# Performance work log

Measured on AMD Instinct MI355X. Metric: run time of the kernel, lower is better.

Reference implementation:

```python
import jax, jax.numpy as jnp
import numpy as np

N = 10000   # total nodes (hits) across events
K = 16      # n_neighbours (excluding self)
F = 64      # input feature dim
H = 128     # hidden width (hard-coded in module)
BIG = 1e9

def _selu(x):
    return jax.nn.selu(x)

def _glorot(key, shape):
    fan_in, fan_out = shape
    s = jnp.sqrt(2.0 / (fan_in + fan_out)).astype(jnp.float32)
    return jax.random.normal(key, shape, dtype=jnp.float32) * s

def setup_inputs() -> dict:
    key = jax.random.key(0)
    ks = jax.random.split(key, 10)
    h = jax.random.normal(ks[0], (N, F), dtype=jnp.float32)
    coords = jax.random.normal(ks[1], (N, 3), dtype=jnp.float32)
    row_splits = jnp.array([0, N // 2, N], dtype=jnp.int32)
    return {
        'h': h, 'coords': coords, 'row_splits': row_splits,
        'W_e1': _glorot(ks[2], (2 * F + 1, H)), 'b_e1': jnp.zeros((H,), jnp.float32),
        'W_e2': _glorot(ks[3], (H, H)), 'b_e2': jnp.zeros((H,), jnp.float32),
        'W_c1': _glorot(ks[4], (H, H)), 'b_c1': jnp.zeros((H,), jnp.float32),
        'W_c2': _glorot(ks[5], (H, 1)), 'b_c2': jnp.zeros((1,), jnp.float32),
        'W_n1': _glorot(ks[6], (H + F, H)), 'b_n1': jnp.zeros((H,), jnp.float32),
        'W_n2': _glorot(ks[7], (H, H)), 'b_n2': jnp.zeros((H,), jnp.float32),
    }

def _knn(coords, row_splits):
    # segment id per node from row_splits (constant)
    n = coords.shape[0]
    seg = jnp.searchsorted(row_splits, jnp.arange(n), side='right') - 1
    nrm = jnp.sum(coords * coords, axis=1)                      # [N]
    d2 = nrm[:, None] + nrm[None, :] - 2.0 * (coords @ coords.T)
    d2 = jnp.maximum(d2, 0.0)
    same = seg[:, None] == seg[None, :]
    d2 = jnp.where(same, d2, BIG)
    negd, idx = jax.lax.top_k(-d2, K + 1)                       # includes self (dist 0)
    dist = jnp.maximum(-negd, 0.0)                              # [N, K+1]
    return idx, dist

def reference(h, coords, row_splits, W_e1, b_e1, W_e2, b_e2, W_c1, b_c1, W_c2, b_c2, W_n1, b_n1, W_n2, b_n2):
    idx, dist = _knn(coords, row_splits)                        # [N,K+1]
    nidx = idx[:, 1:]                                           # [N,K]
    d = dist[:, 1:]                                             # [N,K]
    coord_diff = coords[:, None, :] - coords[idx[:, 1:]]        # [N,K,3]

    hg = h[idx]                                                 # SelectWithDefault gather [N,K+1,F]
    h_self = hg[:, 0, :]                                        # [N,F]
    h_node = jnp.broadcast_to(h_self[:, None, :], (h.shape[0], K, F)).reshape(-1, F)
    h_neig = hg[:, 1:, :].reshape(-1, F)
    radial0 = d.reshape(-1, 1)

    e = jnp.concatenate([radial0, h_node, h_neig], axis=1)      # [N*K, 2F+1]
    e = _selu(e @ W_e1 + b_e1)
    e = _selu(e @ W_e2 + b_e2)                                  # [N*K, H]

    c = _selu(e @ W_c1 + b_c1)
    w = (c @ W_c2 + b_c2).reshape(-1, K, 1)                     # [N,K,1]
    trans = jnp.mean(coord_diff * w, axis=1)                    # [N,3]
    coords_new = coords + trans

    e_sum = e.reshape(-1, K, H).sum(axis=1)                     # [N,H]
    agg = jnp.concatenate([e_sum, h_self], axis=1)              # [N,H+F]
    out = _selu(agg @ W_n1 + b_n1) @ W_n2 + b_n2                # [N,H]
    return out, coords_new, nidx, d
```

## Files before the change

kernel.cpp:

```cpp
#include <hip/hip_runtime.h>
#include <cstdint>

#define KNB 16
#define FDIM 64
#define HDIM 128
#define NPB 8
#define ROWS 128
#define CMAXW 80
#define PADN 5120

typedef unsigned long long ull;
typedef _Float16 f16x8 __attribute__((ext_vector_type(8)));
typedef float    f32x16 __attribute__((ext_vector_type(16)));

__device__ __forceinline__ float selu_f(float x){
    const float a = 1.6732632423543772f, s = 1.0507009873554805f;
    return x > 0.f ? s * x : s * a * (__expf(x) - 1.0f);
}

__device__ __forceinline__ unsigned int pack2(float a, float b){
    union { _Float16 h[2]; unsigned int u; } t;
    t.h[0] = (_Float16)a; t.h[1] = (_Float16)b;
    return t.u;
}

__device__ __forceinline__ f16x8 ldfrag4(const unsigned int* p, unsigned int di){
    union { uint4 q; f16x8 v; } t;
    t.q = *(const uint4*)(p + di);
    return t.v;
}

template<int CTRL>
__device__ __forceinline__ unsigned int dppmin_u32(unsigned int v){
    unsigned int t = (unsigned int)__builtin_amdgcn_update_dpp(
        -1, (int)v, CTRL, 0xF, 0xF, false);
    return t < v ? t : v;
}
__device__ __forceinline__ unsigned int wave_min_u32(unsigned int v){
    v = dppmin_u32<0x111>(v);
    v = dppmin_u32<0x112>(v);
    v = dppmin_u32<0x114>(v);
    v = dppmin_u32<0x118>(v);
    v = dppmin_u32<0x142>(v);
    v = dppmin_u32<0x143>(v);
    return (unsigned int)__builtin_amdgcn_readlane((int)v, 63);
}

__global__ __launch_bounds__(256) void prep_kernel(
    const float* __restrict__ We1, const float* __restrict__ We2,
    const float* __restrict__ Wc1, _Float16* __restrict__ WT,
    const float* __restrict__ coords, float4* __restrict__ c4, int n, int npad)
{
    int b = blockIdx.x;
    if (b < 192){
        int id = b * 256 + threadIdx.x;
        int m  = id >> 14;
        int r  = id & 16383;
        int nn = (r >> 7) & 127;
        int k  = r & 127;
        float v;
        if (m == 0)      v = We1[(k + 1) * 128 + nn];
        else if (m == 1) v = We2[k * 128 + nn];
        else             v = Wc1[k * 128 + nn];
        WT[m * 16384 + nn * 128 + k] = (_Float16)v;
    } else {
        int i = (b - 192) * 256 + threadIdx.x;
        if (i < n){
            float x = coords[3*i], y = coords[3*i+1], z = coords[3*i+2];
            float nrm = __fadd_rn(__fadd_rn(__fmul_rn(x,x), __fmul_rn(y,y)), __fmul_rn(z,z));
            c4[i] = make_float4(x, y, z, nrm);
        } else if (i < npad){
            c4[i] = make_float4(0.f, 0.f, 0.f, __uint_as_float(0x7f800000u));
        }
    }
}

__global__ __launch_bounds__(256) void knn_kernel(
    const float4* __restrict__ c4,
    const int* __restrict__ row_splits, int nseg, int n,
    int* __restrict__ nidx, float* __restrict__ ndist, int* __restrict__ idx0,
    float* __restrict__ out_nidx, float* __restrict__ out_d)
{
    const int lane = threadIdx.x & 63;
    const int wid  = threadIdx.x >> 6;
    const int i    = blockIdx.x * 4 + wid;
    if (i >= n) return;

    int lo = 0, hi = n;
    for (int s = 0; s < nseg; ++s){
        int a = row_splits[s], b = row_splits[s+1];
        if (i >= a && i < b){ lo = a; hi = b; }
    }

    const float4 ci = c4[i];
    const float cx = ci.x, cy = ci.y, cz = ci.z, nrmi = ci.w;

    const int jbase = lo + lane;
    const float FINF = __uint_as_float(0x7f800000u);

    ull m1 = ~0ull, m2 = ~0ull, m3 = ~0ull;

    #define D2_OF(v) __fsub_rn(__fadd_rn(nrmi, (v).w), __fmul_rn(2.0f, \
        __fadd_rn(__fadd_rn(__fmul_rn(cx,(v).x), __fmul_rn(cy,(v).y)), __fmul_rn(cz,(v).z))))
    #define INS(kk) { \
        ull n1 = (kk) < m1 ? (kk) : m1; \
        ull t1 = (kk) < m1 ? m1 : (kk); \
        ull n2 = t1 < m2 ? t1 : m2; \
        ull t2 = t1 < m2 ? m2 : t1; \
        ull n3 = t2 < m3 ? t2 : m3; \
        m1 = n1; m2 = n2; m3 = n3; }

    for (int c0 = 0; c0 < CMAXW; c0 += 8){
        float4 v[8]; int jj[8];
        #pragma unroll
        for (int q = 0; q < 8; ++q){
            jj[q] = jbase + (c0 + q)*64;
            v[q]  = c4[jj[q]];
        }
        #pragma unroll
        for (int q = 0; q < 8; ++q){
            float dv = (jj[q] < hi) ? fmaxf(D2_OF(v[q]), 0.0f) : FINF;
            ull kk = (((ull)__float_as_uint(dv)) << 32) | (unsigned int)jj[q];
            INS(kk)
        }
    }
    int vcnt = 3;

    for (int r = 0; r < KNB + 1; ++r){
        unsigned int h32 = (unsigned int)(m1 >> 32);
        unsigned int l32 = (unsigned int)m1;
        unsigned int wmd = wave_min_u32(h32);
        unsigned int jm  = (h32 == wmd) ? l32 : 0xFFFFFFFFu;
        unsigned int wmj = wave_min_u32(jm);

        bool own = (h32 == wmd) && (l32 == wmj);
        bool need = false;
        if (own){
            int   j  = (int)wmj;
            float dv = __uint_as_float(wmd);
            if (r == 0){
                idx0[i] = j;
            } else {
                int rr = r - 1;
                nidx[i*KNB + rr]     = j;
                ndist[i*KNB + rr]    = dv;
                out_nidx[i*KNB + rr] = (float)j;
                out_d[i*KNB + rr]    = dv;
            }
            m1 = m2; m2 = m3; m3 = ~0ull;
            need = (--vcnt == 0);
        }

        if (__ballot((int)need)){
            if (need){
                ull b = (((ull)wmd) << 32) | wmj;
                m1 = m2 = m3 = ~0ull;
                for (int c = 0; c < CMAXW; ++c){
                    int j = jbase + c*64;
                    float4 v = c4[j];
                    float dv = (j < hi) ? fmaxf(D2_OF(v), 0.0f) : FINF;
                    ull kk = (((ull)__float_as_uint(dv)) << 32) | (unsigned int)j;
                    kk = kk > b ? kk : ~0ull;
                    INS(kk)
                }
                vcnt = 3;
            }
        }
    }
    #undef INS
    #undef D2_OF
}

#define SWZ(row, d) ((unsigned int)(d) ^ ((((unsigned int)(row)) & 7u) << 2))

__global__ __launch_bounds__(256, 2) void egcn_node_kernel(
    const float* __restrict__ h, const float* __restrict__ coords,
    const int* __restrict__ nidx, const float* __restrict__ ndist,
    const int* __restrict__ idx0, const _Float16* __restrict__ WTg,
    const float* __restrict__ W_e1, const float* __restrict__ b_e1,
    const float* __restrict__ b_e2, const float* __restrict__ b_c1,
    const float* __restrict__ W_c2, const float* __restrict__ b_c2,
    float* __restrict__ aggout, float* __restrict__ out_coords, int n)
{
    __shared__ __attribute__((aligned(16))) _Float16 Act[ROWS * 128];
    __shared__ __attribute__((aligned(16))) unsigned int wt[ROWS * 64];
    __shared__ float agg[NPB][HDIM];
    __shared__ float dls[ROWS];
    __shared__ int   nb[ROWS];
    __shared__ int   j0s[NPB];
    __shared__ float wedge[ROWS];

    const int g0  = blockIdx.x * NPB;
    const int tid = threadIdx.x;
    const int lane = tid & 63, wid = tid >> 6;
    const int ln31 = lane & 31, grp = lane >> 5;
    const int rt  = wid;

    if (tid < ROWS){
        int e = min(g0*KNB + tid, n*KNB - 1);
        nb[tid]  = nidx[e];
        dls[tid] = ndist[e];
    }
    if (tid < NPB) j0s[tid] = idx0[min(g0 + tid, n - 1)];
    __syncthreads();

    unsigned int* actd = (unsigned int*)Act;

    {
        int r = tid >> 1, half = tid & 1;
        const float4* hs = (const float4*)(h + (size_t)j0s[r >> 4] * FDIM + half*32);
        const float4* hn = (const float4*)(h + (size_t)nb[r] * FDIM + half*32);
        unsigned int rb = (unsigned int)r * 64;
        uint4 buf[4];
        #pragma unroll
        for (int q = 0; q < 4; ++q){
            float4 a = hs[2*q], b = hs[2*q+1];
            buf[q].x = pack2(a.x,a.y); buf[q].y = pack2(a.z,a.w);
            buf[q].z = pack2(b.x,b.y); buf[q].w = pack2(b.z,b.w);
        }
        #pragma unroll
        for (int q = 0; q < 4; ++q)
            *(uint4*)(actd + rb + SWZ(r, half*16 + 4*q)) = buf[q];
        #pragma unroll
        for (int q = 0; q < 4; ++q){
            float4 a = hn[2*q], b = hn[2*q+1];
            buf[q].x = pack2(a.x,a.y); buf[q].y = pack2(a.z,a.w);
            buf[q].z = pack2(b.x,b.y); buf[q].w = pack2(b.z,b.w);
        }
        #pragma unroll
        for (int q = 0; q < 4; ++q)
            *(uint4*)(actd + rb + SWZ(r, 32 + half*16 + 4*q)) = buf[q];
    }
    auto stage_wt = [&](const _Float16* Wg){
        int nr = tid >> 1, half = tid & 1;
        const uint4* src = (const uint4*)(Wg + nr * 128 + half*64);
        unsigned int rb = (unsigned int)nr * 64;
        #pragma unroll
        for (int q = 0; q < 8; ++q)
            *(uint4*)(wt + rb + SWZ(nr, half*32 + q*4)) = src[q];
    };
    stage_wt(WTg);
    __syncthreads();

    const unsigned int sA    = ((unsigned int)ln31 & 7u) << 2;
    const unsigned int aRow  = (unsigned int)(rt*32 + ln31) * 64;
    const unsigned int bRow0 = (unsigned int)(ln31      ) * 64;
    const unsigned int bRow1 = (unsigned int)(32  + ln31) * 64;
    const unsigned int bRow2 = (unsigned int)(64  + ln31) * 64;
    const unsigned int bRow3 = (unsigned int)(96  + ln31) * 64;

    auto gemm4 = [&](f32x16& A0, f32x16& A1, f32x16& A2, f32x16& A3){
        #pragma unroll
        for (int ks = 0; ks < 8; ++ks){
            const unsigned int o = ((unsigned int)(ks*8 + grp*4)) ^ sA;
            f16x8 af = ldfrag4(actd, aRow + o);
            A0 = __builtin_amdgcn_mfma_f32_32x32x16_f16(af, ldfrag4(wt, bRow0 + o), A0, 0, 0, 0);
            A1 = __builtin_amdgcn_mfma_f32_32x32x16_f16(af, ldfrag4(wt, bRow1 + o), A1, 0, 0, 0);
            A2 = __builtin_amdgcn_mfma_f32_32x32x16_f16(af, ldfrag4(wt, bRow2 + o), A2, 0, 0, 0);
            A3 = __builtin_amdgcn_mfma_f32_32x32x16_f16(af, ldfrag4(wt, bRow3 + o), A3, 0, 0, 0);
        }
    };
    #define ROW_OF(reg) (rt*32 + ((reg)&3) + 8*((reg)>>2) + 4*grp)

    auto act_st = [&](int row, int col, float v){
        unsigned int d = SWZ(row, col >> 1);
        Act[row*128 + (d << 1) + (col & 1)] = (_Float16)v;
    };

    {
        float w00 = W_e1[ln31],      w01 = W_e1[32+ln31];
        float w02 = W_e1[64+ln31],   w03 = W_e1[96+ln31];
        float bz0 = b_e1[ln31],      bz1 = b_e1[32+ln31];
        float bz2 = b_e1[64+ln31],   bz3 = b_e1[96+ln31];
        f32x16 a0, a1, a2, a3;
        #pragma unroll
        for (int reg = 0; reg < 16; ++reg){
            float dv = dls[ROW_OF(reg)];
            a0[reg] = fmaf(dv, w00, bz0);
            a1[reg] = fmaf(dv, w01, bz1);
            a2[reg] = fmaf(dv, w02, bz2);
            a3[reg] = fmaf(dv, w03, bz3);
        }
        gemm4(a0, a1, a2, a3);
        __syncthreads();
        #pragma unroll
        for (int reg = 0; reg < 16; ++reg){
            int row = ROW_OF(reg);
            act_st(row, ln31,      selu_f(a0[reg]));
            act_st(row, 32 + ln31, selu_f(a1[reg]));
            act_st(row, 64 + ln31, selu_f(a2[reg]));
            act_st(row, 96 + ln31, selu_f(a3[reg]));
        }
        stage_wt(WTg + 16384);
        __syncthreads();
    }

    {
        float bz0 = b_e2[ln31],    bz1 = b_e2[32+ln31];
        float bz2 = b_e2[64+ln31], bz3 = b_e2[96+ln31];
        f32x16 a0, a1, a2, a3;
        #pragma unroll
        for (int reg = 0; reg < 16; ++reg){ a0[reg]=bz0; a1[reg]=bz1; a2[reg]=bz2; a3[reg]=bz3; }
        gemm4(a0, a1, a2, a3);
        __syncthreads();
        float e0[16], e1v[16], e2v[16], e3[16];
        float sl0=0.f, sh0=0.f, sl1=0.f, sh1=0.f, sl2=0.f, sh2=0.f, sl3=0.f, sh3=0.f;
        #pragma unroll
        for (int reg = 0; reg < 16; ++reg){
            e0[reg]=selu_f(a0[reg]); e1v[reg]=selu_f(a1[reg]);
            e2v[reg]=selu_f(a2[reg]); e3[reg]=selu_f(a3[reg]);
            if (reg < 8){ sl0+=e0[reg]; sl1+=e1v[reg]; sl2+=e2v[reg]; sl3+=e3[reg]; }
            else        { sh0+=e0[reg]; sh1+=e1v[reg]; sh2+=e2v[reg]; sh3+=e3[reg]; }
        }
        sl0 += __shfl_xor(sl0, 32, 64);  sh0 += __shfl_xor(sh0, 32, 64);
        sl1 += __shfl_xor(sl1, 32, 64);  sh1 += __shfl_xor(sh1, 32, 64);
        sl2 += __shfl_xor(sl2, 32, 64);  sh2 += __shfl_xor(sh2, 32, 64);
        sl3 += __shfl_xor(sl3, 32, 64);  sh3 += __shfl_xor(sh3, 32, 64);
        if (grp == 0){
            agg[rt*2+0][ln31]      = sl0;  agg[rt*2+1][ln31]      = sh0;
            agg[rt*2+0][32 + ln31] = sl1;  agg[rt*2+1][32 + ln31] = sh1;
            agg[rt*2+0][64 + ln31] = sl2;  agg[rt*2+1][64 + ln31] = sh2;
            agg[rt*2+0][96 + ln31] = sl3;  agg[rt*2+1][96 + ln31] = sh3;
        }
        #pragma unroll
        for (int reg = 0; reg < 16; ++reg){
            int row = ROW_OF(reg);
            act_st(row, ln31,      e0[reg]);
            act_st(row, 32 + ln31, e1v[reg]);
            act_st(row, 64 + ln31, e2v[reg]);
            act_st(row, 96 + ln31, e3[reg]);
        }
        stage_wt(WTg + 2*16384);
        __syncthreads();
    }

    {
        float bz0 = b_c1[ln31],    bz1 = b_c1[32+ln31];
        float bz2 = b_c1[64+ln31], bz3 = b_c1[96+ln31];
        f32x16 a0, a1, a2, a3;
        #pragma unroll
        for (int reg = 0; reg < 16; ++reg){ a0[reg]=bz0; a1[reg]=bz1; a2[reg]=bz2; a3[reg]=bz3; }
        gemm4(a0, a1, a2, a3);
        __syncthreads();
        float wc0 = W_c2[ln31],    wc1 = W_c2[32+ln31];
        float wc2 = W_c2[64+ln31], wc3 = W_c2[96+ln31];
        float bc2 = b_c2[0];
        float p[16];
        #pragma unroll
        for (int reg = 0; reg < 16; ++reg)
            p[reg] = selu_f(a0[reg])*wc0 + selu_f(a1[reg])*wc1
                   + selu_f(a2[reg])*wc2 + selu_f(a3[reg])*wc3;
        #pragma unroll
        for (int msk = 16; msk > 0; msk >>= 1){
            #pragma unroll
            for (int reg = 0; reg < 16; ++reg)
                p[reg] += __shfl_xor(p[reg], msk, 64);
        }
        if (ln31 == 0){
            #pragma unroll
            for (int reg = 0; reg < 16; ++reg)
                wedge[ROW_OF(reg)] = bc2 + p[reg];
        }
        __syncthreads();
    }

    if (tid < 3*NPB){
        int nd = tid / 3, c = tid - nd*3;
        int gi = min(g0 + nd, n - 1);
        float ci = coords[3*gi + c];
        float s = 0.f;
        #pragma unroll
        for (int k = 0; k < KNB; ++k){
            int e = nd*KNB + k;
            s += (ci - coords[3*nb[e] + c]) * wedge[e];
        }
        if (g0 + nd < n) out_coords[3*gi + c] = ci + s * (1.0f/KNB);
    }

    for (int s = tid; s < NPB*192; s += 256){
        int nd = s / 192, c = s - nd*192;
        if (g0 + nd < n){
            float v = (c < HDIM) ? agg[nd][c]
                                 : h[(size_t)j0s[nd]*FDIM + (c - HDIM)];
            aggout[(size_t)(g0 + nd)*192 + c] = v;
        }
    }
}

#define NMB 16
__global__ __launch_bounds__(256) void node_mlp_kernel(
    const float* __restrict__ aggin,
    const float* __restrict__ W_n1, const float* __restrict__ b_n1,
    const float* __restrict__ W_n2, const float* __restrict__ b_n2,
    float* __restrict__ out, int n)
{
    __shared__ __attribute__((aligned(16))) float sinT[192][20];
    __shared__ float part[2][NMB][HDIM];

    const int g0  = blockIdx.x * NMB;
    const int tid = threadIdx.x;
    const int o    = tid & 127;
    const int half = tid >> 7;

    for (int s = tid; s < NMB*192; s += 256){
        size_t gidx = (size_t)g0*192 + s;
        size_t lim  = (size_t)n*192 - 1;
        float v = aggin[gidx < lim ? gidx : lim];
        int nd = s / 192, in = s - nd*192;
        sinT[in][nd] = v;
    }
    __syncthreads();

    {
        float a[NMB];
        #pragma unroll
        for (int d = 0; d < NMB; ++d) a[d] = 0.f;
        int in0 = half * 96;
        for (int in = in0; in < in0 + 96; ++in){
            float w = W_n1[in*HDIM + o];
            const float4* sp = (const float4*)&sinT[in][0];
            float4 v0 = sp[0], v1 = sp[1], v2 = sp[2], v3 = sp[3];
            a[0]  = fmaf(v0.x, w, a[0]);  a[1]  = fmaf(v0.y, w, a[1]);
            a[2]  = fmaf(v0.z, w, a[2]);  a[3]  = fmaf(v0.w, w, a[3]);
            a[4]  = fmaf(v1.x, w, a[4]);  a[5]  = fmaf(v1.y, w, a[5]);
            a[6]  = fmaf(v1.z, w, a[6]);  a[7]  = fmaf(v1.w, w, a[7]);
            a[8]  = fmaf(v2.x, w, a[8]);  a[9]  = fmaf(v2.y, w, a[9]);
            a[10] = fmaf(v2.z, w, a[10]); a[11] = fmaf(v2.w, w, a[11]);
            a[12] = fmaf(v3.x, w, a[12]); a[13] = fmaf(v3.y, w, a[13]);
            a[14] = fmaf(v3.z, w, a[14]); a[15] = fmaf(v3.w, w, a[15]);
        }
        #pragma unroll
        for (int d = 0; d < NMB; ++d) part[half][d][o] = a[d];
    }
    __syncthreads();

    for (int s = tid; s < NMB*HDIM; s += 256){
        int nd = s >> 7, o2 = s & 127;
        sinT[o2][nd] = selu_f(part[0][nd][o2] + part[1][nd][o2] + b_n1[o2]);
    }
    __syncthreads();

    {
        float a[NMB];
        #pragma unroll
        for (int d = 0; d < NMB; ++d) a[d] = 0.f;
        int in0 = half * 64;
        for (int in = in0; in < in0 + 64; ++in){
            float w = W_n2[in*HDIM + o];
            const float4* sp = (const float4*)&sinT[in][0];
            float4 v0 = sp[0], v1 = sp[1], v2 = sp[2], v3 = sp[3];
            a[0]  = fmaf(v0.x, w, a[0]);  a[1]  = fmaf(v0.y, w, a[1]);
            a[2]  = fmaf(v0.z, w, a[2]);  a[3]  = fmaf(v0.w, w, a[3]);
            a[4]  = fmaf(v1.x, w, a[4]);  a[5]  = fmaf(v1.y, w, a[5]);
            a[6]  = fmaf(v1.z, w, a[6]);  a[7]  = fmaf(v1.w, w, a[7]);
            a[8]  = fmaf(v2.x, w, a[8]);  a[9]  = fmaf(v2.y, w, a[9]);
            a[10] = fmaf(v2.z, w, a[10]); a[11] = fmaf(v2.w, w, a[11]);
            a[12] = fmaf(v3.x, w, a[12]); a[13] = fmaf(v3.y, w, a[13]);
            a[14] = fmaf(v3.z, w, a[14]); a[15] = fmaf(v3.w, w, a[15]);
        }
        #pragma unroll
        for (int d = 0; d < NMB; ++d) part[half][d][o] = a[d];
    }
    __syncthreads();

    for (int s = tid; s < NMB*HDIM; s += 256){
        int nd = s >> 7, o2 = s & 127;
        if (g0 + nd < n)
            out[(size_t)(g0 + nd)*HDIM + o2] =
                part[0][nd][o2] + part[1][nd][o2] + b_n2[o2];
    }
}

extern "C" void kernel_launch(void* const* d_in, const int* in_sizes, int n_in,
                              void* d_out, int out_size, void* d_ws, size_t ws_size,
                              hipStream_t stream)
{
    const float* h          = (const float*)d_in[0];
    const float* coords     = (const float*)d_in[1];
    const int*   row_splits = (const int*)  d_in[2];
    const float* W_e1 = (const float*)d_in[3];
    const float* b_e1 = (const float*)d_in[4];
    const float* W_e2 = (const float*)d_in[5];
    const float* b_e2 = (const float*)d_in[6];
    const float* W_c1 = (const float*)d_in[7];
    const float* b_c1 = (const float*)d_in[8];
    const float* W_c2 = (const float*)d_in[9];
    const float* b_c2 = (const float*)d_in[10];
    const float* W_n1 = (const float*)d_in[11];
    const float* b_n1 = (const float*)d_in[12];
    const float* W_n2 = (const float*)d_in[13];
    const float* b_n2 = (const float*)d_in[14];

    const int n    = in_sizes[0] / FDIM;
    const int nseg = in_sizes[2] - 1;
    const int npad = n + PADN;

    float* out        = (float*)d_out;
    float* out_coords = out + (size_t)n * HDIM;
    float* out_nidx   = out_coords + (size_t)n * 3;
    float* out_d      = out_nidx + (size_t)n * KNB;

    int*       nidx_i = (int*)d_ws;
    float*     ndist  = (float*)(nidx_i + (size_t)n * KNB);
    int*       idx0   = (int*)(ndist + (size_t)n * KNB);
    _Float16*  WT     = (_Float16*)(idx0 + (size_t)n);
    float*     aggbuf = (float*)(WT + 3 * 16384);
    float4*    c4     = (float4*)(aggbuf + (size_t)n * 192);

    const int prep_blocks = 192 + (npad + 255) / 256;
    prep_kernel<<<prep_blocks, 256, 0, stream>>>(W_e1, W_e2, W_c1, WT,
                                                 coords, c4, n, npad);

    knn_kernel<<<(n + 3) / 4, 256, 0, stream>>>(c4, row_splits, nseg, n,
                                                nidx_i, ndist, idx0, out_nidx, out_d);

    egcn_node_kernel<<<(n + NPB - 1) / NPB, 256, 0, stream>>>(
        h, coords, nidx_i, ndist, idx0, WT,
        W_e1, b_e1, b_e2, b_c1, W_c2, b_c2,
        aggbuf, out_coords, n);

    node_mlp_kernel<<<(n + NMB - 1) / NMB, 256, 0, stream>>>(
        aggbuf, W_n1, b_n1, W_n2, b_n2, out, n);
}
```

Before: 258.9 us.

## Read GEMM weights from global, drop weight LDS staging, use double top-3 keys

The node kernel stops staging each 128x128 fp16 weight matrix into shared memory and has MFMA B fragments loaded straight from global (L2/L1-cached) memory. This frees 32KB of LDS and removes one barrier, and launch bounds are raised to 4 blocks per CU for more occupancy. The kNN kernel also packs distance and index into a double so top-3 insertion uses fmin/fmax instead of 64-bit integer compares. The risk is global load latency on the GEMM inner loop, and register pressure from the higher occupancy target.

```diff
diff --git a/kernel.cpp b/kernel.cpp
--- a/kernel.cpp
+++ b/kernel.cpp
@@ -27,6 +27,12 @@
 __device__ __forceinline__ f16x8 ldfrag4(const unsigned int* p, unsigned int di){
     union { uint4 q; f16x8 v; } t;
     t.q = *(const uint4*)(p + di);
+    return t.v;
+}
+
+__device__ __forceinline__ f16x8 ldg8h(const _Float16* p){
+    union { uint4 q; f16x8 v; } t;
+    t.q = *(const uint4*)p;
     return t.v;
 }
 
@@ -96,18 +102,17 @@
     const float cx = ci.x, cy = ci.y, cz = ci.z, nrmi = ci.w;
 
     const int jbase = lo + lane;
-    const float FINF = __uint_as_float(0x7f800000u);
-
-    ull m1 = ~0ull, m2 = ~0ull, m3 = ~0ull;
+    const float  FINF = __uint_as_float(0x7f800000u);
+    const double DINF = __longlong_as_double(0x7FF0000000000000LL);
+
+    double m1 = DINF, m2 = DINF, m3 = DINF;
 
     #define D2_OF(v) __fsub_rn(__fadd_rn(nrmi, (v).w), __fmul_rn(2.0f, \
         __fadd_rn(__fadd_rn(__fmul_rn(cx,(v).x), __fmul_rn(cy,(v).y)), __fmul_rn(cz,(v).z))))
     #define INS(kk) { \
-        ull n1 = (kk) < m1 ? (kk) : m1; \
-        ull t1 = (kk) < m1 ? m1 : (kk); \
-        ull n2 = t1 < m2 ? t1 : m2; \
-        ull t2 = t1 < m2 ? m2 : t1; \
-        ull n3 = t2 < m3 ? t2 : m3; \
+        double n1 = fmin(kk, m1), t1 = fmax(kk, m1); \
+        double n2 = fmin(t1, m2), t2 = fmax(t1, m2); \
+        double n3 = fmin(t2, m3); \
         m1 = n1; m2 = n2; m3 = n3; }
 
     for (int c0 = 0; c0 < CMAXW; c0 += 8){
@@ -120,15 +125,15 @@
         #pragma unroll
         for (int q = 0; q < 8; ++q){
             float dv = (jj[q] < hi) ? fmaxf(D2_OF(v[q]), 0.0f) : FINF;
-            ull kk = (((ull)__float_as_uint(dv)) << 32) | (unsigned int)jj[q];
+            double kk = __hiloint2double((int)__float_as_uint(dv), jj[q]);
             INS(kk)
         }
     }
     int vcnt = 3;
 
     for (int r = 0; r < KNB + 1; ++r){
-        unsigned int h32 = (unsigned int)(m1 >> 32);
-        unsigned int l32 = (unsigned int)m1;
+        unsigned int h32 = (unsigned int)__double2hiint(m1);
+        unsigned int l32 = (unsigned int)__double2loint(m1);
         unsigned int wmd = wave_min_u32(h32);
         unsigned int jm  = (h32 == wmd) ? l32 : 0xFFFFFFFFu;
         unsigned int wmj = wave_min_u32(jm);
@@ -147,20 +152,20 @@
                 out_nidx[i*KNB + rr] = (float)j;
                 out_d[i*KNB + rr]    = dv;
             }
-            m1 = m2; m2 = m3; m3 = ~0ull;
+            m1 = m2; m2 = m3; m3 = DINF;
             need = (--vcnt == 0);
         }
 
         if (__ballot((int)need)){
             if (need){
-                ull b = (((ull)wmd) << 32) | wmj;
-                m1 = m2 = m3 = ~0ull;
+                double bd = __hiloint2double((int)wmd, (int)wmj);
+                m1 = m2 = m3 = DINF;
                 for (int c = 0; c < CMAXW; ++c){
                     int j = jbase + c*64;
                     float4 v = c4[j];
                     float dv = (j < hi) ? fmaxf(D2_OF(v), 0.0f) : FINF;
-                    ull kk = (((ull)__float_as_uint(dv)) << 32) | (unsigned int)j;
-                    kk = kk > b ? kk : ~0ull;
+                    double kk = __hiloint2double((int)__float_as_uint(dv), j);
+                    kk = (kk > bd) ? kk : DINF;
                     INS(kk)
                 }
                 vcnt = 3;
@@ -173,7 +178,7 @@
 
 #define SWZ(row, d) ((unsigned int)(d) ^ ((((unsigned int)(row)) & 7u) << 2))
 
-__global__ __launch_bounds__(256, 2) void egcn_node_kernel(
+__global__ __launch_bounds__(256, 4) void egcn_node_kernel(
     const float* __restrict__ h, const float* __restrict__ coords,
     const int* __restrict__ nidx, const float* __restrict__ ndist,
     const int* __restrict__ idx0, const _Float16* __restrict__ WTg,
@@ -183,7 +188,6 @@
     float* __restrict__ aggout, float* __restrict__ out_coords, int n)
 {
     __shared__ __attribute__((aligned(16))) _Float16 Act[ROWS * 128];
-    __shared__ __attribute__((aligned(16))) unsigned int wt[ROWS * 64];
     __shared__ float agg[NPB][HDIM];
     __shared__ float dls[ROWS];
     __shared__ int   nb[ROWS];
@@ -231,33 +235,28 @@
         for (int q = 0; q < 4; ++q)
             *(uint4*)(actd + rb + SWZ(r, 32 + half*16 + 4*q)) = buf[q];
     }
-    auto stage_wt = [&](const _Float16* Wg){
-        int nr = tid >> 1, half = tid & 1;
-        const uint4* src = (const uint4*)(Wg + nr * 128 + half*64);
-        unsigned int rb = (unsigned int)nr * 64;
-        #pragma unroll
-        for (int q = 0; q < 8; ++q)
-            *(uint4*)(wt + rb + SWZ(nr, half*32 + q*4)) = src[q];
-    };
-    stage_wt(WTg);
     __syncthreads();
 
-    const unsigned int sA    = ((unsigned int)ln31 & 7u) << 2;
-    const unsigned int aRow  = (unsigned int)(rt*32 + ln31) * 64;
-    const unsigned int bRow0 = (unsigned int)(ln31      ) * 64;
-    const unsigned int bRow1 = (unsigned int)(32  + ln31) * 64;
-    const unsigned int bRow2 = (unsigned int)(64  + ln31) * 64;
-    const unsigned int bRow3 = (unsigned int)(96  + ln31) * 64;
-
-    auto gemm4 = [&](f32x16& A0, f32x16& A1, f32x16& A2, f32x16& A3){
+    const unsigned int sA   = ((unsigned int)ln31 & 7u) << 2;
+    const unsigned int aRow = (unsigned int)(rt*32 + ln31) * 64;
+
+    auto gemm4 = [&](const _Float16* Wb, f32x16& A0, f32x16& A1, f32x16& A2, f32x16& A3){
+        const _Float16* w0 = Wb + (size_t)(ln31      ) * 128 + grp*8;
+        const _Float16* w1 = Wb + (size_t)(32 + ln31 ) * 128 + grp*8;
+        const _Float16* w2 = Wb + (size_t)(64 + ln31 ) * 128 + grp*8;
+        const _Float16* w3 = Wb + (size_t)(96 + ln31 ) * 128 + grp*8;
         #pragma unroll
         for (int ks = 0; ks < 8; ++ks){
             const unsigned int o = ((unsigned int)(ks*8 + grp*4)) ^ sA;
             f16x8 af = ldfrag4(actd, aRow + o);
-            A0 = __builtin_amdgcn_mfma_f32_32x32x16_f16(af, ldfrag4(wt, bRow0 + o), A0, 0, 0, 0);
-            A1 = __builtin_amdgcn_mfma_f32_32x32x16_f16(af, ldfrag4(wt, bRow1 + o), A1, 0, 0, 0);
-            A2 = __builtin_amdgcn_mfma_f32_32x32x16_f16(af, ldfrag4(wt, bRow2 + o), A2, 0, 0, 0);
-            A3 = __builtin_amdgcn_mfma_f32_32x32x16_f16(af, ldfrag4(wt, bRow3 + o), A3, 0, 0, 0);
+            f16x8 b0 = ldg8h(w0 + ks*16);
+            f16x8 b1 = ldg8h(w1 + ks*16);
+            f16x8 b2 = ldg8h(w2 + ks*16);
+            f16x8 b3 = ldg8h(w3 + ks*16);
+            A0 = __builtin_amdgcn_mfma_f32_32x32x16_f16(af, b0, A0, 0, 0, 0);
+            A1 = __builtin_amdgcn_mfma_f32_32x32x16_f16(af, b1, A1, 0, 0, 0);
+            A2 = __builtin_amdgcn_mfma_f32_32x32x16_f16(af, b2, A2, 0, 0, 0);
+            A3 = __builtin_amdgcn_mfma_f32_32x32x16_f16(af, b3, A3, 0, 0, 0);
         }
     };
     #define ROW_OF(reg) (rt*32 + ((reg)&3) + 8*((reg)>>2) + 4*grp)
@@ -281,7 +280,7 @@
             a2[reg] = fmaf(dv, w02, bz2);
             a3[reg] = fmaf(dv, w03, bz3);
         }
-        gemm4(a0, a1, a2, a3);
+        gemm4(WTg, a0, a1, a2, a3);
         __syncthreads();
         #pragma unroll
         for (int reg = 0; reg < 16; ++reg){
@@ -291,7 +290,6 @@
             act_st(row, 64 + ln31, selu_f(a2[reg]));
             act_st(row, 96 + ln31, selu_f(a3[reg]));
         }
-        stage_wt(WTg + 16384);
         __syncthreads();
     }
 
@@ -301,7 +299,7 @@
         f32x16 a0, a1, a2, a3;
         #pragma unroll
         for (int reg = 0; reg < 16; ++reg){ a0[reg]=bz0; a1[reg]=bz1; a2[reg]=bz2; a3[reg]=bz3; }
-        gemm4(a0, a1, a2, a3);
+        gemm4(WTg + 16384, a0, a1, a2, a3);
         __syncthreads();
         float e0[16], e1v[16], e2v[16], e3[16];
         float sl0=0.f, sh0=0.f, sl1=0.f, sh1=0.f, sl2=0.f, sh2=0.f, sl3=0.f, sh3=0.f;
@@ -330,7 +328,6 @@
             act_st(row, 64 + ln31, e2v[reg]);
             act_st(row, 96 + ln31, e3[reg]);
         }
-        stage_wt(WTg + 2*16384);
         __syncthreads();
     }
 
@@ -340,8 +337,7 @@
         f32x16 a0, a1, a2, a3;
         #pragma unroll
         for (int reg = 0; reg < 16; ++reg){ a0[reg]=bz0; a1[reg]=bz1; a2[reg]=bz2; a3[reg]=bz3; }
-        gemm4(a0, a1, a2, a3);
-        __syncthreads();
+        gemm4(WTg + 2*16384, a0, a1, a2, a3);
         float wc0 = W_c2[ln31],    wc1 = W_c2[32+ln31];
         float wc2 = W_c2[64+ln31], wc3 = W_c2[96+ln31];
         float bc2 = b_c2[0];
```

Result: slower. 305.6 us (+18.0%).

## Run node MLP on fp16 MFMA with half-precision aggregate buffer

Applied to the files above, without the earlier changes.

Replaces the scalar-FMA fp32 node MLP with a 32x32x16 fp16 MFMA implementation that processes 128 nodes per block. The W_n1 and W_n2 weights are transposed and converted to fp16 in the prep kernel. The intermediate aggregate buffer is now written as packed fp16, which halves that traffic. This targets the FMA-bound node MLP and its global round-trip, at the cost of fp16 rounding on the activations and weights, and fewer blocks (about 79) that may underfill the GPU.

```diff
diff --git a/kernel.cpp b/kernel.cpp
--- a/kernel.cpp
+++ b/kernel.cpp
@@ -27,6 +27,12 @@
 __device__ __forceinline__ f16x8 ldfrag4(const unsigned int* p, unsigned int di){
     union { uint4 q; f16x8 v; } t;
     t.q = *(const uint4*)(p + di);
+    return t.v;
+}
+
+__device__ __forceinline__ f16x8 ldg8h(const _Float16* p){
+    union { uint4 q; f16x8 v; } t;
+    t.q = *(const uint4*)p;
     return t.v;
 }
 
@@ -46,9 +52,13 @@
     return (unsigned int)__builtin_amdgcn_readlane((int)v, 63);
 }
 
+#define SWZ(row, d) ((unsigned int)(d) ^ ((((unsigned int)(row)) & 7u) << 2))
+
 __global__ __launch_bounds__(256) void prep_kernel(
     const float* __restrict__ We1, const float* __restrict__ We2,
     const float* __restrict__ Wc1, _Float16* __restrict__ WT,
+    const float* __restrict__ Wn1, _Float16* __restrict__ WN1T,
+    const float* __restrict__ Wn2, _Float16* __restrict__ WN2T,
     const float* __restrict__ coords, float4* __restrict__ c4, int n, int npad)
 {
     int b = blockIdx.x;
@@ -63,8 +73,16 @@
         else if (m == 1) v = We2[k * 128 + nn];
         else             v = Wc1[k * 128 + nn];
         WT[m * 16384 + nn * 128 + k] = (_Float16)v;
+    } else if (b < 288){
+        int id = (b - 192) * 256 + threadIdx.x;
+        int nn = id / 192, k = id - nn * 192;
+        WN1T[nn * 192 + k] = (_Float16)Wn1[k * 128 + nn];
+    } else if (b < 352){
+        int id = (b - 288) * 256 + threadIdx.x;
+        int nn = id >> 7, k = id & 127;
+        WN2T[nn * 128 + k] = (_Float16)Wn2[k * 128 + nn];
     } else {
-        int i = (b - 192) * 256 + threadIdx.x;
+        int i = (b - 352) * 256 + threadIdx.x;
         if (i < n){
             float x = coords[3*i], y = coords[3*i+1], z = coords[3*i+2];
             float nrm = __fadd_rn(__fadd_rn(__fmul_rn(x,x), __fmul_rn(y,y)), __fmul_rn(z,z));
@@ -171,8 +189,6 @@
     #undef D2_OF
 }
 
-#define SWZ(row, d) ((unsigned int)(d) ^ ((((unsigned int)(row)) & 7u) << 2))
-
 __global__ __launch_bounds__(256, 2) void egcn_node_kernel(
     const float* __restrict__ h, const float* __restrict__ coords,
     const int* __restrict__ nidx, const float* __restrict__ ndist,
@@ -180,7 +196,7 @@
     const float* __restrict__ W_e1, const float* __restrict__ b_e1,
     const float* __restrict__ b_e2, const float* __restrict__ b_c1,
     const float* __restrict__ W_c2, const float* __restrict__ b_c2,
-    float* __restrict__ aggout, float* __restrict__ out_coords, int n)
+    unsigned int* __restrict__ aggout, float* __restrict__ out_coords, int n)
 {
     __shared__ __attribute__((aligned(16))) _Float16 Act[ROWS * 128];
     __shared__ __attribute__((aligned(16))) unsigned int wt[ROWS * 64];
@@ -377,98 +393,115 @@
         if (g0 + nd < n) out_coords[3*gi + c] = ci + s * (1.0f/KNB);
     }
 
-    for (int s = tid; s < NPB*192; s += 256){
-        int nd = s / 192, c = s - nd*192;
+    for (int s = tid; s < NPB*96; s += 256){
+        int nd = s / 96, c2 = s - nd*96;
         if (g0 + nd < n){
-            float v = (c < HDIM) ? agg[nd][c]
-                                 : h[(size_t)j0s[nd]*FDIM + (c - HDIM)];
-            aggout[(size_t)(g0 + nd)*192 + c] = v;
-        }
-    }
-}
-
-#define NMB 16
-__global__ __launch_bounds__(256) void node_mlp_kernel(
-    const float* __restrict__ aggin,
-    const float* __restrict__ W_n1, const float* __restrict__ b_n1,
-    const float* __restrict__ W_n2, const float* __restrict__ b_n2,
+            int c = c2 * 2;
+            float v0 = (c   < HDIM) ? agg[nd][c]
+                                    : h[(size_t)j0s[nd]*FDIM + (c - HDIM)];
+            float v1 = (c+1 < HDIM) ? agg[nd][c+1]
+                                    : h[(size_t)j0s[nd]*FDIM + (c+1 - HDIM)];
+            aggout[(size_t)(g0 + nd)*96 + c2] = pack2(v0, v1);
+        }
+    }
+}
+
+__global__ __launch_bounds__(256, 2) void node_mlp_kernel(
+    const unsigned int* __restrict__ aggin,
+    const _Float16* __restrict__ WN1T, const float* __restrict__ b_n1,
+    const _Float16* __restrict__ WN2T, const float* __restrict__ b_n2,
     float* __restrict__ out, int n)
 {
-    __shared__ __attribute__((aligned(16))) float sinT[192][20];
-    __shared__ float part[2][NMB][HDIM];
-
-    const int g0  = blockIdx.x * NMB;
+    __shared__ __attribute__((aligned(16))) unsigned int Act[128 * 96];
+    _Float16* acth = (_Float16*)Act;
+
+    const int g0  = blockIdx.x * 128;
     const int tid = threadIdx.x;
-    const int o    = tid & 127;
-    const int half = tid >> 7;
-
-    for (int s = tid; s < NMB*192; s += 256){
-        size_t gidx = (size_t)g0*192 + s;
-        size_t lim  = (size_t)n*192 - 1;
-        float v = aggin[gidx < lim ? gidx : lim];
-        int nd = s / 192, in = s - nd*192;
-        sinT[in][nd] = v;
+    const int lane = tid & 63, wid = tid >> 6;
+    const int ln31 = lane & 31, grp = lane >> 5;
+    const int rt  = wid;
+
+    const int maxch = n * 24 - 1;
+    #pragma unroll
+    for (int q = 0; q < 12; ++q){
+        int ch = q * 256 + tid;
+        int r  = ch / 24, c = ch - r * 24;
+        int gch = min(g0 * 24 + ch, maxch);
+        uint4 v = *(const uint4*)(aggin + (size_t)gch * 4);
+        *(uint4*)(Act + r * 96 + SWZ(r, 4 * c)) = v;
     }
     __syncthreads();
 
+    const unsigned int sA   = ((unsigned int)ln31 & 7u) << 2;
+    const unsigned int aRow = (unsigned int)(rt*32 + ln31) * 96;
+    #define ROW_OF(reg) (rt*32 + ((reg)&3) + 8*((reg)>>2) + 4*grp)
+
+    f32x16 a0, a1, a2, a3;
     {
-        float a[NMB];
-        #pragma unroll
-        for (int d = 0; d < NMB; ++d) a[d] = 0.f;
-        int in0 = half * 96;
-        for (int in = in0; in < in0 + 96; ++in){
-            float w = W_n1[in*HDIM + o];
-            const float4* sp = (const float4*)&sinT[in][0];
-            float4 v0 = sp[0], v1 = sp[1], v2 = sp[2], v3 = sp[3];
-            a[0]  = fmaf(v0.x, w, a[0]);  a[1]  = fmaf(v0.y, w, a[1]);
-            a[2]  = fmaf(v0.z, w, a[2]);  a[3]  = fmaf(v0.w, w, a[3]);
-            a[4]  = fmaf(v1.x, w, a[4]);  a[5]  = fmaf(v1.y, w, a[5]);
-            a[6]  = fmaf(v1.z, w, a[6]);  a[7]  = fmaf(v1.w, w, a[7]);
-            a[8]  = fmaf(v2.x, w, a[8]);  a[9]  = fmaf(v2.y, w, a[9]);
-            a[10] = fmaf(v2.z, w, a[10]); a[11] = fmaf(v2.w, w, a[11]);
-            a[12] = fmaf(v3.x, w, a[12]); a[13] = fmaf(v3.y, w, a[13]);
-            a[14] = fmaf(v3.z, w, a[14]); a[15] = fmaf(v3.w, w, a[15]);
-        }
-        #pragma unroll
-        for (int d = 0; d < NMB; ++d) part[half][d][o] = a[d];
+        float bz0 = b_n1[ln31],    bz1 = b_n1[32+ln31];
+        float bz2 = b_n1[64+ln31], bz3 = b_n1[96+ln31];
+        #pragma unroll
+        for (int reg = 0; reg < 16; ++reg){ a0[reg]=bz0; a1[reg]=bz1; a2[reg]=bz2; a3[reg]=bz3; }
+        const _Float16* w0 = WN1T + (size_t)(ln31      ) * 192 + grp*8;
+        const _Float16* w1 = WN1T + (size_t)(32 + ln31 ) * 192 + grp*8;
+        const _Float16* w2 = WN1T + (size_t)(64 + ln31 ) * 192 + grp*8;
+        const _Float16* w3 = WN1T + (size_t)(96 + ln31 ) * 192 + grp*8;
+        #pragma unroll
+        for (int ks = 0; ks < 12; ++ks){
+            const unsigned int o = ((unsigned int)(ks*8 + grp*4)) ^ sA;
+            f16x8 af = ldfrag4(Act, aRow + o);
+            a0 = __builtin_amdgcn_mfma_f32_32x32x16_f16(af, ldg8h(w0 + ks*16), a0, 0, 0, 0);
+            a1 = __builtin_amdgcn_mfma_f32_32x32x16_f16(af, ldg8h(w1 + ks*16), a1, 0, 0, 0);
+            a2 = __builtin_amdgcn_mfma_f32_32x32x16_f16(af, ldg8h(w2 + ks*16), a2, 0, 0, 0);
+            a3 = __builtin_amdgcn_mfma_f32_32x32x16_f16(af, ldg8h(w3 + ks*16), a3, 0, 0, 0);
+        }
     }
     __syncthreads();
-
-    for (int s = tid; s < NMB*HDIM; s += 256){
-        int nd = s >> 7, o2 = s & 127;
-        sinT[o2][nd] = selu_f(part[0][nd][o2] + part[1][nd][o2] + b_n1[o2]);
+    #pragma unroll
+    for (int reg = 0; reg < 16; ++reg){
+        int row = ROW_OF(reg);
+        #pragma unroll
+        for (int t = 0; t < 4; ++t){
+            int col = t*32 + ln31;
+            float v = (t==0) ? a0[reg] : (t==1) ? a1[reg] : (t==2) ? a2[reg] : a3[reg];
+            unsigned int d = SWZ(row, col >> 1);
+            acth[row*192 + (d << 1) + (col & 1)] = (_Float16)selu_f(v);
+        }
     }
     __syncthreads();
 
     {
-        float a[NMB];
-        #pragma unroll
-        for (int d = 0; d < NMB; ++d) a[d] = 0.f;
-        int in0 = half * 64;
-        for (int in = in0; in < in0 + 64; ++in){
-            float w = W_n2[in*HDIM + o];
-            const float4* sp = (const float4*)&sinT[in][0];
-            float4 v0 = sp[0], v1 = sp[1], v2 = sp[2], v3 = sp[3];
-            a[0]  = fmaf(v0.x, w, a[0]);  a[1]  = fmaf(v0.y, w, a[1]);
-            a[2]  = fmaf(v0.z, w, a[2]);  a[3]  = fmaf(v0.w, w, a[3]);
-            a[4]  = fmaf(v1.x, w, a[4]);  a[5]  = fmaf(v1.y, w, a[5]);
-            a[6]  = fmaf(v1.z, w, a[6]);  a[7]  = fmaf(v1.w, w, a[7]);
-            a[8]  = fmaf(v2.x, w, a[8]);  a[9]  = fmaf(v2.y, w, a[9]);
-            a[10] = fmaf(v2.z, w, a[10]); a[11] = fmaf(v2.w, w, a[11]);
-            a[12] = fmaf(v3.x, w, a[12]); a[13] = fmaf(v3.y, w, a[13]);
-            a[14] = fmaf(v3.z, w, a[14]); a[15] = fmaf(v3.w, w, a[15]);
-        }
-        #pragma unroll
-        for (int d = 0; d < NMB; ++d) part[half][d][o] = a[d];
-    }
-    __syncthreads();
-
-    for (int s = tid; s < NMB*HDIM; s += 256){
-        int nd = s >> 7, o2 = s & 127;
-        if (g0 + nd < n)
-            out[(size_t)(g0 + nd)*HDIM + o2] =
-                part[0][nd][o2] + part[1][nd][o2] + b_n2[o2];
-    }
+        float bz0 = b_n2[ln31],    bz1 = b_n2[32+ln31];
+        float bz2 = b_n2[64+ln31], bz3 = b_n2[96+ln31];
+        #pragma unroll
+        for (int reg = 0; reg < 16; ++reg){ a0[reg]=bz0; a1[reg]=bz1; a2[reg]=bz2; a3[reg]=bz3; }
+        const _Float16* w0 = WN2T + (size_t)(ln31      ) * 128 + grp*8;
+        const _Float16* w1 = WN2T + (size_t)(32 + ln31 ) * 128 + grp*8;
+        const _Float16* w2 = WN2T + (size_t)(64 + ln31 ) * 128 + grp*8;
+        const _Float16* w3 = WN2T + (size_t)(96 + ln31 ) * 128 + grp*8;
+        #pragma unroll
+        for (int ks = 0; ks < 8; ++ks){
+            const unsigned int o = ((unsigned int)(ks*8 + grp*4)) ^ sA;
+            f16x8 af = ldfrag4(Act, aRow + o);
+            a0 = __builtin_amdgcn_mfma_f32_32x32x16_f16(af, ldg8h(w0 + ks*16), a0, 0, 0, 0);
+            a1 = __builtin_amdgcn_mfma_f32_32x32x16_f16(af, ldg8h(w1 + ks*16), a1, 0, 0, 0);
+            a2 = __builtin_amdgcn_mfma_f32_32x32x16_f16(af, ldg8h(w2 + ks*16), a2, 0, 0, 0);
+            a3 = __builtin_amdgcn_mfma_f32_32x32x16_f16(af, ldg8h(w3 + ks*16), a3, 0, 0, 0);
+        }
+    }
+    #pragma unroll
+    for (int reg = 0; reg < 16; ++reg){
+        int row = ROW_OF(reg);
+        int node = g0 + row;
+        if (node < n){
+            float* op = out + (size_t)node * HDIM;
+            op[ln31]      = a0[reg];
+            op[32 + ln31] = a1[reg];
+            op[64 + ln31] = a2[reg];
+            op[96 + ln31] = a3[reg];
+        }
+    }
+    #undef ROW_OF
 }
 
 extern "C" void kernel_launch(void* const* d_in, const int* in_sizes, int n_in,
@@ -500,15 +533,18 @@
     float* out_nidx   = out_coords + (size_t)n * 3;
     float* out_d      = out_nidx + (size_t)n * KNB;
 
-    int*       nidx_i = (int*)d_ws;
-    float*     ndist  = (float*)(nidx_i + (size_t)n * KNB);
-    int*       idx0   = (int*)(ndist + (size_t)n * KNB);
-    _Float16*  WT     = (_Float16*)(idx0 + (size_t)n);
-    float*     aggbuf = (float*)(WT + 3 * 16384);
-    float4*    c4     = (float4*)(aggbuf + (size_t)n * 192);
-
-    const int prep_blocks = 192 + (npad + 255) / 256;
+    int*          nidx_i = (int*)d_ws;
+    float*        ndist  = (float*)(nidx_i + (size_t)n * KNB);
+    int*          idx0   = (int*)(ndist + (size_t)n * KNB);
+    _Float16*     WT     = (_Float16*)(idx0 + (size_t)n);
+    _Float16*     WN1T   = WT + 3 * 16384;
+    _Float16*     WN2T   = WN1T + 128 * 192;
+    unsigned int* aggbuf = (unsigned int*)(WN2T + 128 * 128);
+    float4*       c4     = (float4*)(aggbuf + (size_t)n * 96);
+
+    const int prep_blocks = 352 + (npad + 255) / 256;
     prep_kernel<<<prep_blocks, 256, 0, stream>>>(W_e1, W_e2, W_c1, WT,
+                                                 W_n1, WN1T, W_n2, WN2T,
                                                  coords, c4, n, npad);
 
     knn_kernel<<<(n + 3) / 4, 256, 0, stream>>>(c4, row_splits, nseg, n,
@@ -519,6 +555,6 @@
         W_e1, b_e1, b_e2, b_c1, W_c2, b_c2,
         aggbuf, out_coords, n);
 
-    node_mlp_kernel<<<(n + NMB - 1) / NMB, 256, 0, stream>>>(
-        aggbuf, W_n1, b_n1, W_n2, b_n2, out, n);
-}
+    node_mlp_kernel<<<(n + 127) / 128, 256, 0, stream>>>(
+        aggbuf, WN1T, b_n1, WN2T, b_n2, out, n);
+}
```

Result: faster. 248.5 us (-4.0%).
